# Optimization experiments

Hardware: AMD Instinct MI355X
Metric: run time of the kernel (lower is better)

## Reference

```python
import jax, jax.numpy as jnp
import numpy as np
import math

B, NIN, DIM, QK, GS, L, BINS = 512, 128, 512, 128, 32, 2, 100
HID = int(DIM * 2.0)
G = NIN // GS
ROT = 32  # rotary dim = min(32, query_key_dim)
EPS = 1e-5


def setup_inputs() -> dict:
    key = jax.random.key(0)
    ks = jax.random.split(key, 8)
    r = jax.random.normal
    return {
        "tokens": jax.random.randint(ks[0], (B, NIN), 0, BINS),
        "emb": r(ks[1], (NIN, BINS, DIM), jnp.float32) * 0.02,
        "pos_emb": r(ks[2], (NIN, DIM), jnp.float32) * 0.01,
        "norm_g": jnp.ones((L,), jnp.float32),
        "Wh": r(ks[3], (L, DIM, 2 * HID), jnp.float32) / math.sqrt(DIM),
        "bh": jnp.zeros((L, 2 * HID), jnp.float32),
        "Wqk": r(ks[4], (L, DIM, QK), jnp.float32) / math.sqrt(DIM),
        "bqk": jnp.zeros((L, QK), jnp.float32),
        "gamma": r(ks[5], (L, 4, QK), jnp.float32) * 0.02,
        "beta": jnp.zeros((L, 4, QK), jnp.float32),
        "rp": r(ks[6], (L, 32), jnp.float32) * 0.02,
        "Wout": r(ks[7], (L, HID, DIM), jnp.float32) / math.sqrt(HID),
        "bout": jnp.zeros((L, DIM), jnp.float32),
        "ln_g": jnp.ones((DIM,), jnp.float32),
        "ln_b": jnp.zeros((DIM,), jnp.float32),
    }


def _t5_buckets(n, num_buckets=32, max_distance=128):
    # causal T5 relative position buckets, computed statically
    pos = np.arange(n)
    rel = pos[None, :] - pos[:, None]
    neg = np.maximum(-rel, 0)
    max_exact = num_buckets // 2
    vl = max_exact + (np.log(np.maximum(neg, 1) / max_exact) / np.log(max_distance / max_exact) * (num_buckets - max_exact)).astype(np.int64)
    vl = np.minimum(vl, num_buckets - 1)
    return jnp.asarray(np.where(neg < max_exact, neg, vl))


def _rotary_cos_sin(n):
    inv = 1.0 / (10000.0 ** (np.arange(0, ROT, 2) / ROT))
    f = np.einsum('i,j->ij', np.arange(n), inv)  # [n, ROT/2]
    f = np.repeat(f, 2, axis=-1)                 # interleaved-pair freqs [n, ROT]
    return jnp.asarray(np.cos(f), jnp.float32), jnp.asarray(np.sin(f), jnp.float32)


def _apply_rotary(x, cos, sin):
    xr, xp = x[..., :ROT], x[..., ROT:]
    x2 = xr.reshape(*xr.shape[:-1], ROT // 2, 2)
    rh = jnp.stack((-x2[..., 1], x2[..., 0]), axis=-1).reshape(xr.shape)
    return jnp.concatenate([xr * cos + rh * sin, xp], axis=-1)


def reference(tokens, emb, pos_emb, norm_g, Wh, bh, Wqk, bqk, gamma, beta, rp, Wout, bout, ln_g, ln_b):
    # per-column embedding lookup + positional embedding
    x = emb[jnp.arange(NIN)[None, :], tokens] + pos_emb  # [B, NIN, DIM]
    buckets = _t5_buckets(GS)
    cos, sin = _rotary_cos_sin(NIN)
    t5_scale = QK ** 0.5
    causal_mask = jnp.triu(jnp.ones((GS, GS), bool), 1)

    def grp(t):
        return t.reshape(B, G, GS, t.shape[-1])

    def layer(h, p):
        ng, Wh_l, bh_l, Wqk_l, bqk_l, gm, bt, rp_l, Wo_l, bo_l = p
        # ScaleNorm
        nrm = jnp.linalg.norm(h, axis=-1, keepdims=True) * DIM ** -0.5
        nx = h / jnp.maximum(nrm, EPS) * ng
        # shift_tokens: shift first half of features by one position
        xs, xp = nx[..., :DIM // 2], nx[..., DIM // 2:]
        xs = jnp.pad(xs, ((0, 0), (1, 0), (0, 0)))[:, :-1]
        nx = jnp.concatenate([xs, xp], axis=-1)
        hid = jax.nn.silu(nx @ Wh_l + bh_l)
        v, gate = hid[..., :HID], hid[..., HID:]
        qk = jax.nn.silu(nx @ Wqk_l + bqk_l)
        qs = qk[..., None, :] * gm + bt  # [B, NIN, 4, QK]
        quad_q = _apply_rotary(qs[..., 0, :], cos, sin)
        lin_q = _apply_rotary(qs[..., 1, :], cos, sin)
        quad_k = _apply_rotary(qs[..., 2, :], cos, sin)
        lin_k = _apply_rotary(qs[..., 3, :], cos, sin)
        qq, lq, kk, lk, vg = map(grp, (quad_q, lin_q, quad_k, lin_k, v))
        # grouped quadratic attention with ReLU^2 attn fn and T5 rel-pos bias
        sim = jnp.einsum('bgid,bgjd->bgij', qq, kk) / GS + rp_l[buckets] * t5_scale
        attn = jnp.square(jax.nn.relu(sim))
        attn = jnp.where(causal_mask, 0.0, attn)
        quad_out = jnp.einsum('bgij,bgje->bgie', attn, vg)
        # causal linear attention across groups (shifted cumsum of kv stats)
        lin_kv = jnp.einsum('bgnd,bgne->bgde', lk, vg) / GS
        lin_kv = jnp.cumsum(lin_kv, axis=1)
        lin_kv = jnp.pad(lin_kv, ((0, 0), (1, 0), (0, 0), (0, 0)))[:, :-1]
        lin_out = jnp.einsum('bgde,bgnd->bgne', lin_kv, lq)
        out = gate * (quad_out + lin_out).reshape(B, NIN, HID)
        return out @ Wo_l + bo_l + h, None

    x, _ = jax.lax.scan(layer, x, (norm_g, Wh, bh, Wqk, bqk, gamma, beta, rp, Wout, bout))
    mu = x.mean(-1, keepdims=True)
    var = x.var(-1, keepdims=True)
    return (x - mu) / jnp.sqrt(var + EPS) * ln_g + ln_b
```

## Files before the change

kernel.cpp:

```cpp
#include <hip/hip_runtime.h>
#include <hip/hip_bf16.h>
#include <math.h>
#include <stdint.h>

#define BB   512
#define NIN  128
#define DIMD 512
#define QKD  128
#define GSZ  32
#define GRP  4
#define HID  1024
#define HID2 2048
#define NFUSE 2176
#define ROT  32
#define NLAYER 2
#define EPSF 1e-5f
#define BINS 100

typedef __bf16 bf16x8 __attribute__((ext_vector_type(8)));
typedef float  f32x4  __attribute__((ext_vector_type(4)));
typedef float  f32x16 __attribute__((ext_vector_type(16)));

__device__ __forceinline__ unsigned short f2bf(float f) {
    union { float f; uint32_t u; } v; v.f = f;
    return (unsigned short)((v.u + 0x7FFFu + ((v.u >> 16) & 1u)) >> 16);
}
__device__ __forceinline__ float bf2f(unsigned short h) {
    union { uint32_t u; float f; } v; v.u = ((uint32_t)h) << 16;
    return v.f;
}

__global__ void k_embed(const int* __restrict__ tokens, const float* __restrict__ emb,
                        const float* __restrict__ pos, float* __restrict__ h) {
    int bn = blockIdx.x;
    int n  = bn % NIN;
    int tok = tokens[bn];
    const float4* e4 = (const float4*)(emb + ((size_t)n * BINS + tok) * DIMD);
    const float4* p4 = (const float4*)(pos + (size_t)n * DIMD);
    float4* h4 = (float4*)(h + (size_t)bn * DIMD);
    int t = threadIdx.x;
    float4 a = e4[t], b = p4[t];
    h4[t] = make_float4(a.x + b.x, a.y + b.y, a.z + b.z, a.w + b.w);
}

__global__ void k_nxf(const float* __restrict__ h, unsigned short* __restrict__ nx,
                      const float* __restrict__ ngp) {
    int bn = blockIdx.x; int n = bn % NIN;
    int t = threadIdx.x;
    float4 v = ((const float4*)(h + (size_t)bn * DIMD))[t];
    float sq = v.x * v.x + v.y * v.y + v.z * v.z + v.w * v.w;
    __shared__ float red[2];
    #pragma unroll
    for (int o = 32; o; o >>= 1) sq += __shfl_down(sq, o);
    int lane = t & 63, w = t >> 6;
    if (lane == 0) red[w] = sq;
    __syncthreads();
    float s = red[0] + red[1];
    float nrm = sqrtf(s) * (1.0f / sqrtf((float)DIMD));
    float sc = ngp[0] / fmaxf(nrm, EPSF);
    ushort4 o = make_ushort4(f2bf(v.x * sc), f2bf(v.y * sc), f2bf(v.z * sc), f2bf(v.w * sc));
    if (t < 64) {
        if (n == 0)
            ((ushort4*)(nx + (size_t)bn * DIMD))[t] = make_ushort4(0, 0, 0, 0);
        if (n != NIN - 1)
            ((ushort4*)(nx + (size_t)(bn + 1) * DIMD))[t] = o;
    } else {
        ((ushort4*)(nx + (size_t)bn * DIMD))[t] = o;
    }
}

__global__ void k_wcast(const float* __restrict__ W, unsigned short* __restrict__ Wt,
                        int K, int N) {
    int idx = blockIdx.x * 256 + threadIdx.x;
    int total = N * (K / 8);
    if (idx >= total) return;
    int kb = idx / N, n = idx % N;
    #pragma unroll
    for (int j = 0; j < 8; ++j)
        Wt[(size_t)n * K + kb * 8 + j] = f2bf(W[(size_t)(kb * 8 + j) * N + n]);
}

#define GLOAD_LDS(gp, lp) __builtin_amdgcn_global_load_lds( \
    (const __attribute__((address_space(1))) uint32_t*)(gp), \
    (__attribute__((address_space(3))) uint32_t*)(lp), 16, 0, 0)

__global__ __launch_bounds__(256) void k_gemm_f(
        const unsigned short* __restrict__ A,
        const unsigned short* __restrict__ Bt,
        const float* __restrict__ bias0,
        const float* __restrict__ bias1,
        float* __restrict__ Cf,
        unsigned short* __restrict__ vTp,
        unsigned short* __restrict__ gatep,
        int M, int N, int K) {
    __shared__ unsigned short As[128 * 32];
    __shared__ unsigned short Bs[128 * 32];
    const int tid = threadIdx.x;

    int flat = blockIdx.y * gridDim.x + blockIdx.x;
    int nwg  = gridDim.x * gridDim.y;
    int q = nwg >> 3, r = nwg & 7;
    int xcd = flat & 7, idx = flat >> 3;
    int swz = (xcd < r ? xcd * (q + 1) : r * (q + 1) + (xcd - r) * q) + idx;
    const int bxi = swz % gridDim.x, byi = swz / gridDim.x;
    const int bm = byi * 128, bn = bxi * 128;

    const int lane = tid & 63, wave = tid >> 6;
    const int wm = (wave >> 1) * 64, wn = (wave & 1) * 64;
    const int l15 = lane & 15, l4 = lane >> 4;

    f32x4 acc[4][4];
    #pragma unroll
    for (int i = 0; i < 4; ++i)
        #pragma unroll
        for (int j = 0; j < 4; ++j) acc[i][j] = (f32x4){0.f, 0.f, 0.f, 0.f};

    const int rowA = tid >> 2;
    const int colO = (tid & 3) * 16;
    const int colS = colO ^ ((rowA & 3) << 4);
    const char* gA = (const char*)(A  + (size_t)(bm + rowA) * K) + colS;
    const char* gB = (const char*)(Bt + (size_t)(bn + rowA) * K) + colS;
    const size_t stride64 = (size_t)64 * K * 2;
    unsigned short* ldsA = As + tid * 8;
    unsigned short* ldsB = Bs + tid * 8;

    for (int k0 = 0; k0 < K; k0 += 32) {
        GLOAD_LDS(gA + (size_t)k0 * 2,            ldsA);
        GLOAD_LDS(gA + (size_t)k0 * 2 + stride64, ldsA + 2048);
        GLOAD_LDS(gB + (size_t)k0 * 2,            ldsB);
        GLOAD_LDS(gB + (size_t)k0 * 2 + stride64, ldsB + 2048);
        asm volatile("s_waitcnt vmcnt(0)" ::: "memory");
        __syncthreads();

        bf16x8 af[4], bfr[4];
        #pragma unroll
        for (int f = 0; f < 4; ++f) {
            int rA = wm + f * 16 + l15;
            int rB = wn + f * 16 + l15;
            af[f]  = *(const bf16x8*)&As[rA * 32 + ((l4 ^ (rA & 3)) << 3)];
            bfr[f] = *(const bf16x8*)&Bs[rB * 32 + ((l4 ^ (rB & 3)) << 3)];
        }
        #pragma unroll
        for (int i = 0; i < 4; ++i)
            #pragma unroll
            for (int j = 0; j < 4; ++j)
                acc[i][j] = __builtin_amdgcn_mfma_f32_16x16x32_bf16(af[i], bfr[j], acc[i][j], 0, 0, 0);
        __syncthreads();
    }

    #pragma unroll
    for (int i = 0; i < 4; ++i) {
        const int n0 = wm + i * 16 + l4 * 4;
        #pragma unroll
        for (int j = 0; j < 4; ++j) {
            const int col = bn + wn + j * 16 + l15;
            float bsv = (col < 2 * HID) ? bias0[col] : bias1[col - 2 * HID];
            float vv[4];
            #pragma unroll
            for (int rr = 0; rr < 4; ++rr) {
                float v = acc[i][j][rr] + bsv;
                vv[rr] = v / (1.0f + __expf(-v));
            }
            if (col < HID) {
                ushort4 o = make_ushort4(f2bf(vv[0]), f2bf(vv[1]), f2bf(vv[2]), f2bf(vv[3]));
                *(ushort4*)&vTp[((size_t)byi * HID + col) * NIN + n0] = o;
            } else if (col < 2 * HID) {
                #pragma unroll
                for (int rr = 0; rr < 4; ++rr)
                    gatep[(size_t)(bm + n0 + rr) * HID + (col - HID)] = f2bf(vv[rr]);
            } else {
                #pragma unroll
                for (int rr = 0; rr < 4; ++rr)
                    Cf[(size_t)(bm + n0 + rr) * QKD + (col - 2 * HID)] = vv[rr];
            }
        }
    }
}

__global__ __launch_bounds__(256, 2) void k_gemm_o(
        const unsigned short* __restrict__ A,
        const unsigned short* __restrict__ Bt,
        const float* __restrict__ bias0,
        const float* __restrict__ resid,
        float* __restrict__ Cf,
        int M, int N, int K) {
    __shared__ unsigned short As[2][256 * 32];
    __shared__ unsigned short Bs[2][128 * 32];
    const int tid = threadIdx.x;

    int flat = blockIdx.y * gridDim.x + blockIdx.x;
    int nwg  = gridDim.x * gridDim.y;
    int q = nwg >> 3, r = nwg & 7;
    int xcd = flat & 7, idx = flat >> 3;
    int swz = (xcd < r ? xcd * (q + 1) : r * (q + 1) + (xcd - r) * q) + idx;
    const int bxi = swz % gridDim.x, byi = swz / gridDim.x;
    const int bm = byi * 256, bn = bxi * 128;

    const int lane = tid & 63, wave = tid >> 6;
    const int l15 = lane & 15, l4 = lane >> 4;

    f32x4 acc[4][8];
    #pragma unroll
    for (int i = 0; i < 4; ++i)
        #pragma unroll
        for (int j = 0; j < 8; ++j) acc[i][j] = (f32x4){0.f, 0.f, 0.f, 0.f};

    const int rowA = tid >> 2;
    const int colO = (tid & 3) * 16;
    const int colS = colO ^ ((rowA & 3) << 4);
    const char* gA = (const char*)(A  + (size_t)(bm + rowA) * K) + colS;
    const char* gB = (const char*)(Bt + (size_t)(bn + rowA) * K) + colS;
    const size_t stride64 = (size_t)64 * K * 2;
    unsigned short* dA0 = &As[0][tid * 8];
    unsigned short* dA1 = &As[1][tid * 8];
    unsigned short* dB0 = &Bs[0][tid * 8];
    unsigned short* dB1 = &Bs[1][tid * 8];

    #define STAGE2(dA, dB, k0) do { \
        const char* sA_ = gA + (size_t)(k0) * 2; \
        const char* sB_ = gB + (size_t)(k0) * 2; \
        GLOAD_LDS(sA_,                 (dA)); \
        GLOAD_LDS(sA_ +     stride64,  (dA) + 2048); \
        GLOAD_LDS(sA_ + 2 * stride64,  (dA) + 4096); \
        GLOAD_LDS(sA_ + 3 * stride64,  (dA) + 6144); \
        GLOAD_LDS(sB_,                 (dB)); \
        GLOAD_LDS(sB_ +     stride64,  (dB) + 2048); \
    } while (0)

    STAGE2(dA0, dB0, 0);
    asm volatile("s_waitcnt vmcnt(0)" ::: "memory");
    __syncthreads();

    const int NIT = K / 32;
    int bufc = 0;
    for (int it = 0; it < NIT; ++it) {
        if (it + 1 < NIT) {
            if (bufc == 0) STAGE2(dA1, dB1, (it + 1) * 32);
            else           STAGE2(dA0, dB0, (it + 1) * 32);
        }
        const unsigned short* Ab = As[bufc];
        const unsigned short* Bb = Bs[bufc];
        bf16x8 af[4], bfr[8];
        #pragma unroll
        for (int f = 0; f < 4; ++f) {
            int rA = wave * 64 + f * 16 + l15;
            af[f] = *(const bf16x8*)&Ab[rA * 32 + ((l4 ^ (rA & 3)) << 3)];
        }
        #pragma unroll
        for (int c = 0; c < 8; ++c) {
            int rB = c * 16 + l15;
            bfr[c] = *(const bf16x8*)&Bb[rB * 32 + ((l4 ^ (rB & 3)) << 3)];
        }
        #pragma unroll
        for (int f = 0; f < 4; ++f)
            #pragma unroll
            for (int c = 0; c < 8; ++c)
                acc[f][c] = __builtin_amdgcn_mfma_f32_16x16x32_bf16(af[f], bfr[c], acc[f][c], 0, 0, 0);
        asm volatile("s_waitcnt vmcnt(0)" ::: "memory");
        __syncthreads();
        bufc ^= 1;
    }
    #undef STAGE2

    #pragma unroll
    for (int f = 0; f < 4; ++f) {
        const int n0 = wave * 64 + f * 16 + l4 * 4;
        #pragma unroll
        for (int c = 0; c < 8; ++c) {
            const int col = bn + c * 16 + l15;
            float bsv = bias0[col];
            #pragma unroll
            for (int rr = 0; rr < 4; ++rr) {
                size_t row = bm + n0 + rr;
                Cf[row * N + col] = acc[f][c][rr] + bsv + resid[row * N + col];
            }
        }
    }
}

__global__ void k_cossin(float* __restrict__ cosb, float* __restrict__ sinb) {
    int idx = blockIdx.x * 256 + threadIdx.x;
    if (idx >= NIN * 16) return;
    int n = idx / 16, i = idx % 16;
    double inv = pow(10000.0, -(double)(2 * i) / (double)ROT);
    double f = (double)n * inv;
    cosb[idx] = (float)cos(f);
    sinb[idx] = (float)sin(f);
}

__global__ void k_rot(const float* __restrict__ qk, const float* __restrict__ gm,
                      const float* __restrict__ bt, const float* __restrict__ cosb,
                      const float* __restrict__ sinb, unsigned short* __restrict__ q4) {
    int bn = blockIdx.x; int n = bn % NIN;
    int d = threadIdx.x;
    float x = qk[(size_t)bn * QKD + d];
    float xp0 = 0.f;
    int dp = d ^ 1;
    if (d < ROT) xp0 = qk[(size_t)bn * QKD + dp];
    #pragma unroll
    for (int c = 0; c < 4; ++c) {
        float val = x * gm[c * QKD + d] + bt[c * QKD + d];
        float outv;
        if (d < ROT) {
            int i = d >> 1;
            float cs = cosb[n * 16 + i], sn = sinb[n * 16 + i];
            float xp = xp0 * gm[c * QKD + dp] + bt[c * QKD + dp];
            outv = ((d & 1) == 0) ? (val * cs - xp * sn) : (val * cs + xp * sn);
        } else outv = val;
        q4[((size_t)bn * 4 + c) * QKD + d] = f2bf(outv);
    }
}

__global__ __launch_bounds__(256) void k_attn2(
        const unsigned short* __restrict__ q4,
        const unsigned short* __restrict__ gatep,
        const unsigned short* __restrict__ vT,
        const float* __restrict__ rp,
        unsigned short* __restrict__ attn_out) {
    int et = blockIdx.x, b = blockIdx.y;
    int tid = threadIdx.x, wave = tid >> 6, lane = tid & 63;
    int l31 = lane & 31, lhi = lane >> 5;

    __shared__ unsigned short S[32][136];
    __shared__ float rps_d[32];
    if (tid < 32) {
        int d = tid, bucket;
        if (d < 16) bucket = d;
        else {
            bucket = 16 + (int)(logf((float)d * (1.0f / 16.0f)) * (16.0f / logf(8.0f)));
            if (bucket > 31) bucket = 31;
        }
        rps_d[tid] = rp[bucket] * sqrtf((float)QKD);
    }
    __syncthreads();

    size_t bbase = (size_t)b * NIN;
    int e0 = et * 256 + wave * 64;
    const unsigned short* vbase = vT + (size_t)b * HID * NIN;

    for (int g = 0; g < GRP; ++g) {
        if (wave <= g) {
            int gp = wave;
            bool quad = (gp == g);
            const unsigned short* Qb = q4 + ((bbase + g  * 32 + l31) * 4 + (quad ? 0 : 1)) * QKD;
            const unsigned short* Kb = q4 + ((bbase + gp * 32 + l31) * 4 + (quad ? 2 : 3)) * QKD;
            f32x16 sa = {};
            #pragma unroll
            for (int kk = 0; kk < 8; ++kk) {
                bf16x8 aq = *(const bf16x8*)(Qb + kk * 16 + lhi * 8);
                bf16x8 bk = *(const bf16x8*)(Kb + kk * 16 + lhi * 8);
                sa = __builtin_amdgcn_mfma_f32_32x32x16_bf16(aq, bk, sa, 0, 0, 0);
            }
            int j = l31;
            #pragma unroll
            for (int r = 0; r < 16; ++r) {
                int i = (r & 3) + 8 * (r >> 2) + 4 * lhi;
                float s = sa[r] * (1.0f / GSZ);
                if (quad) {
                    if (j > i) s = 0.f;
                    else {
                        s += rps_d[i - j];
                        s = fmaxf(s, 0.f);
                        s = s * s;
                    }
                }
                S[i][gp * 32 + j] = f2bf(s);
            }
        }
        __syncthreads();

        f32x16 o0 = {}, o1 = {};
        int KT = 2 * (g + 1);
        for (int kk = 0; kk < KT; ++kk) {
            int k0 = kk * 16 + lhi * 8;
            bf16x8 af = *(const bf16x8*)&S[l31][k0];
            bf16x8 b0 = *(const bf16x8*)(vbase + (size_t)(e0 + l31) * NIN + k0);
            bf16x8 b1 = *(const bf16x8*)(vbase + (size_t)(e0 + 32 + l31) * NIN + k0);
            o0 = __builtin_amdgcn_mfma_f32_32x32x16_bf16(af, b0, o0, 0, 0, 0);
            o1 = __builtin_amdgcn_mfma_f32_32x32x16_bf16(af, b1, o1, 0, 0, 0);
        }
        __syncthreads();

        int ea = e0 + l31, eb = e0 + 32 + l31;
        #pragma unroll
        for (int r = 0; r < 16; ++r) {
            int i = (r & 3) + 8 * (r >> 2) + 4 * lhi;
            size_t row = bbase + g * 32 + i;
            float ga = bf2f(gatep[row * HID + ea]);
            float gb = bf2f(gatep[row * HID + eb]);
            attn_out[row * HID + ea] = f2bf(ga * o0[r]);
            attn_out[row * HID + eb] = f2bf(gb * o1[r]);
        }
    }
}

__global__ void k_ln(const float* __restrict__ h, const float* __restrict__ lng,
                     const float* __restrict__ lnb, float* __restrict__ out) {
    int bn = blockIdx.x;
    int t = threadIdx.x;
    const float4* r4 = (const float4*)(h + (size_t)bn * DIMD);
    float4 v = r4[t];
    float s  = v.x + v.y + v.z + v.w;
    float sq = v.x * v.x + v.y * v.y + v.z * v.z + v.w * v.w;
    __shared__ float red[4];
    #pragma unroll
    for (int o = 32; o; o >>= 1) { s += __shfl_down(s, o); sq += __shfl_down(sq, o); }
    int lane = t & 63, w = t >> 6;
    if (lane == 0) { red[w] = s; red[2 + w] = sq; }
    __syncthreads();
    float mu  = (red[0] + red[1]) * (1.0f / DIMD);
    float var = (red[2] + red[3]) * (1.0f / DIMD) - mu * mu;
    float rstd = 1.0f / sqrtf(var + EPSF);
    float4 gg = ((const float4*)lng)[t];
    float4 bb = ((const float4*)lnb)[t];
    float4 o;
    o.x = (v.x - mu) * rstd * gg.x + bb.x;
    o.y = (v.y - mu) * rstd * gg.y + bb.y;
    o.z = (v.z - mu) * rstd * gg.z + bb.z;
    o.w = (v.w - mu) * rstd * gg.w + bb.w;
    ((float4*)(out + (size_t)bn * DIMD))[t] = o;
}

extern "C" void kernel_launch(void* const* d_in, const int* in_sizes, int n_in,
                              void* d_out, int out_size, void* d_ws, size_t ws_size,
                              hipStream_t stream) {
    const int*   tokens = (const int*)d_in[0];
    const float* emb    = (const float*)d_in[1];
    const float* pos    = (const float*)d_in[2];
    const float* norm_g = (const float*)d_in[3];
    const float* Wh     = (const float*)d_in[4];
    const float* bh     = (const float*)d_in[5];
    const float* Wqk    = (const float*)d_in[6];
    const float* bqk    = (const float*)d_in[7];
    const float* gamma  = (const float*)d_in[8];
    const float* beta   = (const float*)d_in[9];
    const float* rp     = (const float*)d_in[10];
    const float* Wout   = (const float*)d_in[11];
    const float* bout   = (const float*)d_in[12];
    const float* lng    = (const float*)d_in[13];
    const float* lnb    = (const float*)d_in[14];

    float* h  = (float*)d_out;
    float* ws = (float*)d_ws;

    size_t off = 0;
    float* cosb  = ws + off; off += NIN * 16;
    float* sinb  = ws + off; off += NIN * 16;
    unsigned short* whqkT = (unsigned short*)(ws + off); off += (size_t)NLAYER * NFUSE * DIMD / 2;
    unsigned short* woutT = (unsigned short*)(ws + off); off += (size_t)NLAYER * DIMD * HID / 2;
    off = (off + 63) & ~(size_t)63;
    const size_t fixedFloats = off;

    const size_t wsFloats = ws_size / sizeof(float);
    const size_t perBatch = (size_t)NIN * (DIMD / 2 + HID / 2 + HID / 2 + QKD + DIMD / 2 + HID / 2);
    int CB = BB;
    while (CB > 2 && fixedFloats + (size_t)CB * perBatch + 64 > wsFloats) CB >>= 1;

    unsigned short* nx    = (unsigned short*)(ws + off); off += (size_t)CB * NIN * DIMD / 2;
    unsigned short* vT    = (unsigned short*)(ws + off); off += (size_t)CB * HID * NIN / 2;
    unsigned short* gateB = (unsigned short*)(ws + off); off += (size_t)CB * NIN * HID / 2;
    float*          qk    = ws + off;                    off += (size_t)CB * NIN * QKD;
    unsigned short* q4    = (unsigned short*)(ws + off); off += (size_t)CB * NIN * DIMD / 2;
    unsigned short* attnB = (unsigned short*)(ws + off); off += (size_t)CB * NIN * HID / 2;

    const int BN_ = BB * NIN;

    k_cossin<<<8, 256, 0, stream>>>(cosb, sinb);
    k_embed<<<BN_, 128, 0, stream>>>(tokens, emb, pos, h);

    for (int l = 0; l < NLAYER; ++l) {
        unsigned short* whqkT_l = whqkT + (size_t)l * NFUSE * DIMD;
        k_wcast<<<(HID2 * DIMD / 8 + 255) / 256, 256, 0, stream>>>(
            Wh + (size_t)l * DIMD * HID2,  whqkT_l, DIMD, HID2);
        k_wcast<<<(QKD * DIMD / 8 + 255) / 256, 256, 0, stream>>>(
            Wqk + (size_t)l * DIMD * QKD,  whqkT_l + (size_t)HID2 * DIMD, DIMD, QKD);
        k_wcast<<<(DIMD * HID / 8 + 255) / 256, 256, 0, stream>>>(
            Wout + (size_t)l * HID * DIMD, woutT + (size_t)l * DIMD * HID, HID, DIMD);
    }

    for (int l = 0; l < NLAYER; ++l) {
        const float* bh_l  = bh   + (size_t)l * HID2;
        const float* bqk_l = bqk  + (size_t)l * QKD;
        const float* gm_l  = gamma+ (size_t)l * 4 * QKD;
        const float* bt_l  = beta + (size_t)l * 4 * QKD;
        const float* rp_l  = rp   + (size_t)l * 32;
        const float* bo_l  = bout + (size_t)l * DIMD;
        const unsigned short* whqkT_l = whqkT + (size_t)l * NFUSE * DIMD;
        const unsigned short* woutT_l = woutT + (size_t)l * DIMD * HID;

        for (int c0 = 0; c0 < BB; c0 += CB) {
            const int rowsC = CB * NIN;
            float* h_c = h + (size_t)c0 * NIN * DIMD;

            k_nxf<<<rowsC, 128, 0, stream>>>(h_c, nx, norm_g + l);

            dim3 g1(NFUSE / 128, rowsC / 128);
            k_gemm_f<<<g1, 256, 0, stream>>>(nx, whqkT_l, bh_l, bqk_l,
                                             qk, vT, gateB, rowsC, NFUSE, DIMD);

            k_rot<<<rowsC, 128, 0, stream>>>(qk, gm_l, bt_l, cosb, sinb, q4);

            dim3 ga(HID / 256, CB);
            k_attn2<<<ga, 256, 0, stream>>>(q4, gateB, vT, rp_l, attnB);

            dim3 g3(DIMD / 128, rowsC / 256);
            k_gemm_o<<<g3, 256, 0, stream>>>(attnB, woutT_l, bo_l, h_c, h_c,
                                             rowsC, DIMD, HID);
        }
    }

    k_ln<<<BN_, 128, 0, stream>>>(h, lng, lnb, (float*)d_out);
}
```

Measured before the change: 1.383 ms.

## Widen GEMM K-tile to 64 and drop double buffering in output GEMM

Both GEMM kernels now stage 64-wide K slices into LDS per iteration instead of 32, using an 8-way XOR swizzle. This halves the number of load/barrier rounds per tile. The output GEMM also drops its two-stage double buffer and becomes a single buffer at the same LDS footprint, so global loads no longer overlap MFMA work. Fewer barriers are traded against lost prefetch overlap.

After: 1.411 ms. Within noise of the previous version (+2.0%).

```diff
diff --git a/kernel.cpp b/kernel.cpp
--- a/kernel.cpp
+++ b/kernel.cpp
@@ -93,8 +93,8 @@
         unsigned short* __restrict__ vTp,
         unsigned short* __restrict__ gatep,
         int M, int N, int K) {
-    __shared__ unsigned short As[128 * 32];
-    __shared__ unsigned short Bs[128 * 32];
+    __shared__ unsigned short As[128 * 64];
+    __shared__ unsigned short Bs[128 * 64];
     const int tid = threadIdx.x;
 
     int flat = blockIdx.y * gridDim.x + blockIdx.x;
@@ -115,36 +115,44 @@
         #pragma unroll
         for (int j = 0; j < 4; ++j) acc[i][j] = (f32x4){0.f, 0.f, 0.f, 0.f};
 
-    const int rowA = tid >> 2;
-    const int colO = (tid & 3) * 16;
-    const int colS = colO ^ ((rowA & 3) << 4);
+    const int rowA = tid >> 3;
+    const int colS = ((tid & 7) << 4) ^ ((rowA & 7) << 4);
     const char* gA = (const char*)(A  + (size_t)(bm + rowA) * K) + colS;
     const char* gB = (const char*)(Bt + (size_t)(bn + rowA) * K) + colS;
-    const size_t stride64 = (size_t)64 * K * 2;
+    const size_t stride32 = (size_t)32 * K * 2;
     unsigned short* ldsA = As + tid * 8;
     unsigned short* ldsB = Bs + tid * 8;
 
-    for (int k0 = 0; k0 < K; k0 += 32) {
-        GLOAD_LDS(gA + (size_t)k0 * 2,            ldsA);
-        GLOAD_LDS(gA + (size_t)k0 * 2 + stride64, ldsA + 2048);
-        GLOAD_LDS(gB + (size_t)k0 * 2,            ldsB);
-        GLOAD_LDS(gB + (size_t)k0 * 2 + stride64, ldsB + 2048);
+    for (int k0 = 0; k0 < K; k0 += 64) {
+        const char* sA = gA + (size_t)k0 * 2;
+        const char* sB = gB + (size_t)k0 * 2;
+        GLOAD_LDS(sA,                 ldsA);
+        GLOAD_LDS(sA +     stride32,  ldsA + 2048);
+        GLOAD_LDS(sA + 2 * stride32,  ldsA + 4096);
+        GLOAD_LDS(sA + 3 * stride32,  ldsA + 6144);
+        GLOAD_LDS(sB,                 ldsB);
+        GLOAD_LDS(sB +     stride32,  ldsB + 2048);
+        GLOAD_LDS(sB + 2 * stride32,  ldsB + 4096);
+        GLOAD_LDS(sB + 3 * stride32,  ldsB + 6144);
         asm volatile("s_waitcnt vmcnt(0)" ::: "memory");
         __syncthreads();
 
-        bf16x8 af[4], bfr[4];
-        #pragma unroll
-        for (int f = 0; f < 4; ++f) {
-            int rA = wm + f * 16 + l15;
-            int rB = wn + f * 16 + l15;
-            af[f]  = *(const bf16x8*)&As[rA * 32 + ((l4 ^ (rA & 3)) << 3)];
-            bfr[f] = *(const bf16x8*)&Bs[rB * 32 + ((l4 ^ (rB & 3)) << 3)];
-        }
-        #pragma unroll
-        for (int i = 0; i < 4; ++i)
-            #pragma unroll
-            for (int j = 0; j < 4; ++j)
-                acc[i][j] = __builtin_amdgcn_mfma_f32_16x16x32_bf16(af[i], bfr[j], acc[i][j], 0, 0, 0);
+        #pragma unroll
+        for (int ks = 0; ks < 2; ++ks) {
+            bf16x8 af[4], bfr[4];
+            #pragma unroll
+            for (int f = 0; f < 4; ++f) {
+                int rA = wm + f * 16 + l15;
+                int rB = wn + f * 16 + l15;
+                af[f]  = *(const bf16x8*)&As[rA * 64 + (((ks * 4 + l4) ^ (rA & 7)) << 3)];
+                bfr[f] = *(const bf16x8*)&Bs[rB * 64 + (((ks * 4 + l4) ^ (rB & 7)) << 3)];
+            }
+            #pragma unroll
+            for (int i = 0; i < 4; ++i)
+                #pragma unroll
+                for (int j = 0; j < 4; ++j)
+                    acc[i][j] = __builtin_amdgcn_mfma_f32_16x16x32_bf16(af[i], bfr[j], acc[i][j], 0, 0, 0);
+        }
         __syncthreads();
     }
 
@@ -184,8 +192,8 @@
         const float* __restrict__ resid,
         float* __restrict__ Cf,
         int M, int N, int K) {
-    __shared__ unsigned short As[2][256 * 32];
-    __shared__ unsigned short Bs[2][128 * 32];
+    __shared__ unsigned short As[256 * 64];
+    __shared__ unsigned short Bs[128 * 64];
     const int tid = threadIdx.x;
 
     int flat = blockIdx.y * gridDim.x + blockIdx.x;
@@ -205,62 +213,47 @@
         #pragma unroll
         for (int j = 0; j < 8; ++j) acc[i][j] = (f32x4){0.f, 0.f, 0.f, 0.f};
 
-    const int rowA = tid >> 2;
-    const int colO = (tid & 3) * 16;
-    const int colS = colO ^ ((rowA & 3) << 4);
+    const int rowA = tid >> 3;
+    const int colS = ((tid & 7) << 4) ^ ((rowA & 7) << 4);
     const char* gA = (const char*)(A  + (size_t)(bm + rowA) * K) + colS;
     const char* gB = (const char*)(Bt + (size_t)(bn + rowA) * K) + colS;
-    const size_t stride64 = (size_t)64 * K * 2;
-    unsigned short* dA0 = &As[0][tid * 8];
-    unsigned short* dA1 = &As[1][tid * 8];
-    unsigned short* dB0 = &Bs[0][tid * 8];
-    unsigned short* dB1 = &Bs[1][tid * 8];
-
-    #define STAGE2(dA, dB, k0) do { \
-        const char* sA_ = gA + (size_t)(k0) * 2; \
-        const char* sB_ = gB + (size_t)(k0) * 2; \
-        GLOAD_LDS(sA_,                 (dA)); \
-        GLOAD_LDS(sA_ +     stride64,  (dA) + 2048); \
-        GLOAD_LDS(sA_ + 2 * stride64,  (dA) + 4096); \
-        GLOAD_LDS(sA_ + 3 * stride64,  (dA) + 6144); \
-        GLOAD_LDS(sB_,                 (dB)); \
-        GLOAD_LDS(sB_ +     stride64,  (dB) + 2048); \
-    } while (0)
-
-    STAGE2(dA0, dB0, 0);
-    asm volatile("s_waitcnt vmcnt(0)" ::: "memory");
-    __syncthreads();
-
-    const int NIT = K / 32;
-    int bufc = 0;
-    for (int it = 0; it < NIT; ++it) {
-        if (it + 1 < NIT) {
-            if (bufc == 0) STAGE2(dA1, dB1, (it + 1) * 32);
-            else           STAGE2(dA0, dB0, (it + 1) * 32);
-        }
-        const unsigned short* Ab = As[bufc];
-        const unsigned short* Bb = Bs[bufc];
-        bf16x8 af[4], bfr[8];
-        #pragma unroll
-        for (int f = 0; f < 4; ++f) {
-            int rA = wave * 64 + f * 16 + l15;
-            af[f] = *(const bf16x8*)&Ab[rA * 32 + ((l4 ^ (rA & 3)) << 3)];
-        }
-        #pragma unroll
-        for (int c = 0; c < 8; ++c) {
-            int rB = c * 16 + l15;
-            bfr[c] = *(const bf16x8*)&Bb[rB * 32 + ((l4 ^ (rB & 3)) << 3)];
-        }
-        #pragma unroll
-        for (int f = 0; f < 4; ++f)
-            #pragma unroll
-            for (int c = 0; c < 8; ++c)
-                acc[f][c] = __builtin_amdgcn_mfma_f32_16x16x32_bf16(af[f], bfr[c], acc[f][c], 0, 0, 0);
+    const size_t stride32 = (size_t)32 * K * 2;
+    unsigned short* ldsA = As + tid * 8;
+    unsigned short* ldsB = Bs + tid * 8;
+
+    for (int k0 = 0; k0 < K; k0 += 64) {
+        const char* sA = gA + (size_t)k0 * 2;
+        const char* sB = gB + (size_t)k0 * 2;
+        #pragma unroll
+        for (int i = 0; i < 8; ++i)
+            GLOAD_LDS(sA + i * stride32, ldsA + i * 2048);
+        #pragma unroll
+        for (int i = 0; i < 4; ++i)
+            GLOAD_LDS(sB + i * stride32, ldsB + i * 2048);
         asm volatile("s_waitcnt vmcnt(0)" ::: "memory");
         __syncthreads();
-        bufc ^= 1;
-    }
-    #undef STAGE2
+
+        #pragma unroll
+        for (int ks = 0; ks < 2; ++ks) {
+            bf16x8 af[4], bfr[8];
+            #pragma unroll
+            for (int f = 0; f < 4; ++f) {
+                int rA = wave * 64 + f * 16 + l15;
+                af[f] = *(const bf16x8*)&As[rA * 64 + (((ks * 4 + l4) ^ (rA & 7)) << 3)];
+            }
+            #pragma unroll
+            for (int c = 0; c < 8; ++c) {
+                int rB = c * 16 + l15;
+                bfr[c] = *(const bf16x8*)&Bs[rB * 64 + (((ks * 4 + l4) ^ (rB & 7)) << 3)];
+            }
+            #pragma unroll
+            for (int f = 0; f < 4; ++f)
+                #pragma unroll
+                for (int c = 0; c < 8; ++c)
+                    acc[f][c] = __builtin_amdgcn_mfma_f32_16x16x32_bf16(af[f], bfr[c], acc[f][c], 0, 0, 0);
+        }
+        __syncthreads();
+    }
 
     #pragma unroll
     for (int f = 0; f < 4; ++f) {
```

## Double-buffer LDS tiles in fused GEMM to overlap global loads with MFMA

Applied to the files above, without the earlier changes.

Splits the shared-memory A/B tiles into two buffers and prefetches the tile two steps ahead with direct global-to-LDS loads. Waits are partial (vmcnt(4)), with explicit barriers around the fragment reads, so memory latency can hide behind the MFMA work. It also drops the XOR swizzle on LDS addresses, which may bring back LDS bank conflicts on the fragment reads. The LDS footprint doubles per block.

Result: faster. 1.348 ms (median of 3 runs) (-2.5%).

```diff
diff --git a/kernel.cpp b/kernel.cpp
--- a/kernel.cpp
+++ b/kernel.cpp
@@ -93,8 +93,8 @@
         unsigned short* __restrict__ vTp,
         unsigned short* __restrict__ gatep,
         int M, int N, int K) {
-    __shared__ unsigned short As[128 * 32];
-    __shared__ unsigned short Bs[128 * 32];
+    __shared__ unsigned short As[2][128 * 32];
+    __shared__ unsigned short Bs[2][128 * 32];
     const int tid = threadIdx.x;
 
     int flat = blockIdx.y * gridDim.x + blockIdx.x;
@@ -116,37 +116,50 @@
         for (int j = 0; j < 4; ++j) acc[i][j] = (f32x4){0.f, 0.f, 0.f, 0.f};
 
     const int rowA = tid >> 2;
-    const int colO = (tid & 3) * 16;
-    const int colS = colO ^ ((rowA & 3) << 4);
-    const char* gA = (const char*)(A  + (size_t)(bm + rowA) * K) + colS;
-    const char* gB = (const char*)(Bt + (size_t)(bn + rowA) * K) + colS;
+    const int colB = (tid & 3) * 16;
+    const char* gA = (const char*)(A  + (size_t)(bm + rowA) * K) + colB;
+    const char* gB = (const char*)(Bt + (size_t)(bn + rowA) * K) + colB;
     const size_t stride64 = (size_t)64 * K * 2;
-    unsigned short* ldsA = As + tid * 8;
-    unsigned short* ldsB = Bs + tid * 8;
-
-    for (int k0 = 0; k0 < K; k0 += 32) {
-        GLOAD_LDS(gA + (size_t)k0 * 2,            ldsA);
-        GLOAD_LDS(gA + (size_t)k0 * 2 + stride64, ldsA + 2048);
-        GLOAD_LDS(gB + (size_t)k0 * 2,            ldsB);
-        GLOAD_LDS(gB + (size_t)k0 * 2 + stride64, ldsB + 2048);
-        asm volatile("s_waitcnt vmcnt(0)" ::: "memory");
-        __syncthreads();
+
+    #define STAGEF(bi, k0) do { \
+        const char* sA_ = gA + (size_t)(k0) * 2; \
+        const char* sB_ = gB + (size_t)(k0) * 2; \
+        GLOAD_LDS(sA_,            &As[bi][tid * 8]); \
+        GLOAD_LDS(sA_ + stride64, &As[bi][tid * 8 + 2048]); \
+        GLOAD_LDS(sB_,            &Bs[bi][tid * 8]); \
+        GLOAD_LDS(sB_ + stride64, &Bs[bi][tid * 8 + 2048]); \
+    } while (0)
+
+    const int NIT = K / 32;
+    STAGEF(0, 0);
+    STAGEF(1, 32);
+
+    for (int t = 0; t < NIT; ++t) {
+        const int cur = t & 1;
+        if (t + 1 < NIT) asm volatile("s_waitcnt vmcnt(4)" ::: "memory");
+        else             asm volatile("s_waitcnt vmcnt(0)" ::: "memory");
+        __builtin_amdgcn_s_barrier();
+        __builtin_amdgcn_sched_barrier(0);
 
         bf16x8 af[4], bfr[4];
         #pragma unroll
         for (int f = 0; f < 4; ++f) {
-            int rA = wm + f * 16 + l15;
-            int rB = wn + f * 16 + l15;
-            af[f]  = *(const bf16x8*)&As[rA * 32 + ((l4 ^ (rA & 3)) << 3)];
-            bfr[f] = *(const bf16x8*)&Bs[rB * 32 + ((l4 ^ (rB & 3)) << 3)];
-        }
+            af[f]  = *(const bf16x8*)&As[cur][(wm + f * 16 + l15) * 32 + l4 * 8];
+            bfr[f] = *(const bf16x8*)&Bs[cur][(wn + f * 16 + l15) * 32 + l4 * 8];
+        }
+        asm volatile("s_waitcnt lgkmcnt(0)" ::: "memory");
+        __builtin_amdgcn_sched_barrier(0);
+        __builtin_amdgcn_s_barrier();
+        __builtin_amdgcn_sched_barrier(0);
+        if (t + 2 < NIT) STAGEF(cur, (t + 2) * 32);
+
         #pragma unroll
         for (int i = 0; i < 4; ++i)
             #pragma unroll
             for (int j = 0; j < 4; ++j)
                 acc[i][j] = __builtin_amdgcn_mfma_f32_16x16x32_bf16(af[i], bfr[j], acc[i][j], 0, 0, 0);
-        __syncthreads();
-    }
+    }
+    #undef STAGEF
 
     #pragma unroll
     for (int i = 0; i < 4; ++i) {
```
